# Performance work log

Hardware: AMD Instinct MI355X
Metric: run time of the kernel (lower is better)

The kernel has to match this reference:

```python
import jax, jax.numpy as jnp
import numpy as np

N, NFEAT, NHID, NHEADS, NCLASS = 4096, 64, 64, 4, 64
ALPHA = 0.2        # LeakyReLU negative slope
NEG = -9.0e15      # mask value from the torch code (-9e15)


def _xavier(key, shape, gain=1.414):
    fan_in, fan_out = shape[-2] if len(shape) > 1 else shape[-1], shape[-1]
    if len(shape) == 1:
        fan_in, fan_out = shape[0], 1
    bound = gain * np.sqrt(6.0 / (fan_in + fan_out))
    return jax.random.uniform(key, shape, jnp.float32, -bound, bound)


def setup_inputs() -> dict:
    key = jax.random.key(0)
    ks = jax.random.split(key, 6)
    x = jax.random.normal(ks[0], (N, NFEAT), jnp.float32)
    # sparse-ish adjacency mask with self loops (adj > 0 gating in torch code)
    adj = jax.random.bernoulli(ks[1], 0.02, (N, N)) | jnp.eye(N, dtype=bool)
    W_heads = _xavier(ks[2], (NHEADS, NFEAT, NHID))                  # per-head W
    a_heads = _xavier(ks[3], (NHEADS, 2 * NHID))                     # per-head a (flattened [2F',1])
    W_out = _xavier(ks[4], (NHEADS * NHID, NCLASS))
    a_out = _xavier(ks[5], (2 * NCLASS,))
    return {"x": x, "W_heads": W_heads, "a_heads": a_heads,
            "W_out": W_out, "a_out": a_out, "adj": adj}


def gat_layer(x, adj, W, a, concat):
    # h: [N, F']
    h = x @ W
    Fp = h.shape[-1]
    # e_ij = leakyrelu(a[:F'].h_i + a[F':].h_j)  == torch's cat([h_i, h_j]) @ a
    f1 = h @ a[:Fp]                 # [N]
    f2 = h @ a[Fp:]                 # [N]
    e = jax.nn.leaky_relu(f1[:, None] + f2[None, :], ALPHA)   # [N, N]
    att = jax.nn.softmax(jnp.where(adj, e, NEG), axis=1)      # row softmax over neighbors
    hp = att @ h                    # [N, F']
    return jax.nn.elu(hp) if concat else hp


def reference(x, W_heads, a_heads, W_out, a_out, adj):
    # multi-head GAT with concat (dropout omitted: eval mode)
    heads = jax.vmap(lambda W, a: gat_layer(x, adj, W, a, True))(W_heads, a_heads)  # [H, N, F']
    hcat = jnp.transpose(heads, (1, 0, 2)).reshape(x.shape[0], NHEADS * NHID)       # [N, H*F']
    out = gat_layer(hcat, adj, W_out, a_out, False)                                  # [N, nclass]
    return out
```

## Files before the change

kernel.cpp:

```cpp
#include <hip/hip_runtime.h>
#include <hip/hip_fp16.h>

#define N 4096
#define CAP 160
#define ALPHA 0.2f

__device__ __forceinline__ float wred_sum(float v) {
#pragma unroll
  for (int o = 32; o > 0; o >>= 1) v += __shfl_xor(v, o, 64);
  return v;
}

__device__ __forceinline__ float4 h4_to_f4(float2 raw) {
  union { float2 f2; __half2 h2[2]; } u;
  u.f2 = raw;
  float2 lo = __half22float2(u.h2[0]);
  float2 hi = __half22float2(u.h2[1]);
  return make_float4(lo.x, lo.y, hi.x, hi.y);
}

__global__ void stage1_k(const void* __restrict__ adjv, const float* __restrict__ x,
                         const float* __restrict__ W, const float* __restrict__ a,
                         int* __restrict__ cnt, int* __restrict__ cols,
                         __half* __restrict__ h1, float* __restrict__ f1h,
                         float* __restrict__ f2h) {
  __shared__ float Ws[64 * 64];
  __shared__ float xs[4][64];
  __shared__ int csh;
  int bid = blockIdx.x;
  int tid = threadIdx.x;
  int lane = tid & 63;
  if (bid < N) {
    int i = bid;
    if (tid == 0) csh = 0;
    __syncthreads();
    int* mycols = cols + (size_t)i * CAP;
    const unsigned char* adjB = (const unsigned char*)adjv;
    bool byteLayout = (adjB[(size_t)N + 1] == 1);
    unsigned long long lt = (lane == 0) ? 0ull : (~0ull >> (64 - lane));
    if (!byteLayout) {
      const int4* row = (const int4*)((const int*)adjv + (size_t)i * N);
      int4 v[4];
#pragma unroll
      for (int it = 0; it < 4; ++it) v[it] = row[tid + it * 256];
#pragma unroll
      for (int it = 0; it < 4; ++it) {
        int b = (tid + it * 256) * 4;
        unsigned long long m0 = __ballot(v[it].x != 0);
        unsigned long long m1 = __ballot(v[it].y != 0);
        unsigned long long m2 = __ballot(v[it].z != 0);
        unsigned long long m3 = __ballot(v[it].w != 0);
        int c0 = __popcll(m0), c1 = __popcll(m1), c2 = __popcll(m2);
        int total = c0 + c1 + c2 + __popcll(m3);
        int wb = 0;
        if (lane == 0 && total) wb = atomicAdd(&csh, total);
        wb = __shfl(wb, 0, 64);
        if (v[it].x) { int p = wb + __popcll(m0 & lt); if (p < CAP) mycols[p] = b; }
        if (v[it].y) { int p = wb + c0 + __popcll(m1 & lt); if (p < CAP) mycols[p] = b + 1; }
        if (v[it].z) { int p = wb + c0 + c1 + __popcll(m2 & lt); if (p < CAP) mycols[p] = b + 2; }
        if (v[it].w) { int p = wb + c0 + c1 + c2 + __popcll(m3 & lt); if (p < CAP) mycols[p] = b + 3; }
      }
    } else {
      const unsigned int* row = (const unsigned int*)(adjB + (size_t)i * N);
      unsigned int v[4];
#pragma unroll
      for (int it = 0; it < 4; ++it) v[it] = row[tid + it * 256];
#pragma unroll
      for (int it = 0; it < 4; ++it) {
        int b = (tid + it * 256) * 4;
        unsigned long long m0 = __ballot((v[it] & 0xffu) != 0);
        unsigned long long m1 = __ballot((v[it] & 0xff00u) != 0);
        unsigned long long m2 = __ballot((v[it] & 0xff0000u) != 0);
        unsigned long long m3 = __ballot((v[it] & 0xff000000u) != 0);
        int c0 = __popcll(m0), c1 = __popcll(m1), c2 = __popcll(m2);
        int total = c0 + c1 + c2 + __popcll(m3);
        int wb = 0;
        if (lane == 0 && total) wb = atomicAdd(&csh, total);
        wb = __shfl(wb, 0, 64);
        if (v[it] & 0xffu) { int p = wb + __popcll(m0 & lt); if (p < CAP) mycols[p] = b; }
        if (v[it] & 0xff00u) { int p = wb + c0 + __popcll(m1 & lt); if (p < CAP) mycols[p] = b + 1; }
        if (v[it] & 0xff0000u) { int p = wb + c0 + c1 + __popcll(m2 & lt); if (p < CAP) mycols[p] = b + 2; }
        if (v[it] & 0xff000000u) { int p = wb + c0 + c1 + c2 + __popcll(m3 & lt); if (p < CAP) mycols[p] = b + 3; }
      }
    }
    __syncthreads();
    if (tid == 0) cnt[i] = min(csh, CAP);
  } else {
    int u = bid - N;
    int h = u & 3;
    int r = tid >> 6, f = lane;
    int n = (u >> 2) * 4 + r;
    const float4* W4 = (const float4*)(W + h * 4096);
    float4* Ws4 = (float4*)Ws;
    for (int t = tid; t < 1024; t += 256) Ws4[t] = W4[t];
    xs[r][f] = x[(size_t)n * 64 + f];
    __syncthreads();
    float acc = 0.f;
#pragma unroll
    for (int k = 0; k < 64; ++k) acc = fmaf(xs[r][k], Ws[k * 64 + f], acc);
    h1[((size_t)h * N + n) * 64 + f] = __float2half(acc);
    float s1 = wred_sum(acc * a[h * 128 + f]);
    float s2 = wred_sum(acc * a[h * 128 + 64 + f]);
    if (f == 0) { f1h[n * 4 + h] = s1; f2h[n * 4 + h] = s2; }
  }
}

__global__ void attn1_gemm_k(const int* __restrict__ cnt, const int* __restrict__ cols,
                             const __half* __restrict__ h1,
                             const float* __restrict__ f1g,
                             const float* __restrict__ f2g,
                             const float* __restrict__ Wout,
                             const float* __restrict__ aout,
                             __half* __restrict__ h2, float* __restrict__ f1o,
                             float* __restrict__ f2o) {
  int i = blockIdx.x;
  int tid = threadIdx.x;
  int w = tid >> 6, lane = tid & 63;
  __shared__ int cS[CAP];
  __shared__ float pS[4][CAP];
  __shared__ float red[4][4];
  __shared__ float sDinv[4];
  __shared__ float hrow[256];
  __shared__ float4 part4[4][16];
  int c = cnt[i];
  for (int k = tid; k < c; k += 256) cS[k] = cols[(size_t)i * CAP + k];
  __syncthreads();
  float4 t1 = ((const float4*)f1g)[i];
  float f1i[4] = {t1.x, t1.y, t1.z, t1.w};
  float dloc[4] = {0.f, 0.f, 0.f, 0.f};
  for (int k = tid; k < c; k += 256) {
    float4 t2 = ((const float4*)f2g)[cS[k]];
    float f2v[4] = {t2.x, t2.y, t2.z, t2.w};
#pragma unroll
    for (int h = 0; h < 4; ++h) {
      float s = f1i[h] + f2v[h];
      s = s > 0.f ? s : ALPHA * s;
      float p = __expf(s);
      pS[h][k] = p;
      dloc[h] += p;
    }
  }
#pragma unroll
  for (int h = 0; h < 4; ++h) {
    float d = wred_sum(dloc[h]);
    if (lane == 0) red[w][h] = d;
  }
  __syncthreads();
  if (tid < 4) {
    float d = red[0][tid] + red[1][tid] + red[2][tid] + red[3][tid];
    sDinv[tid] = (c > 0) ? 1.f / d : 0.f;
  }
  __syncthreads();
  int g = lane >> 4, ff = lane & 15, h = w;
  const __half* hb = h1 + ((size_t)h * N) * 64;
  float4 aA = {0.f, 0.f, 0.f, 0.f}, aB = aA, aC = aA, aD = aA;
#pragma unroll 2
  for (int k0 = 0; k0 < c; k0 += 16) {
    int kA = k0 + g, kB = k0 + 4 + g, kC = k0 + 8 + g, kD = k0 + 12 + g;
    bool oA = kA < c, oB = kB < c, oC = kC < c, oD = kD < c;
    int jA = oA ? cS[kA] : 0, jB = oB ? cS[kB] : 0;
    int jC = oC ? cS[kC] : 0, jD = oD ? cS[kD] : 0;
    float pA = oA ? pS[h][kA] : 0.f, pB = oB ? pS[h][kB] : 0.f;
    float pC = oC ? pS[h][kC] : 0.f, pD = oD ? pS[h][kD] : 0.f;
    float2 rA = *(const float2*)(hb + (size_t)jA * 64 + ff * 4);
    float2 rB = *(const float2*)(hb + (size_t)jB * 64 + ff * 4);
    float2 rC = *(const float2*)(hb + (size_t)jC * 64 + ff * 4);
    float2 rD = *(const float2*)(hb + (size_t)jD * 64 + ff * 4);
    float4 vA = h4_to_f4(rA), vB = h4_to_f4(rB);
    float4 vC = h4_to_f4(rC), vD = h4_to_f4(rD);
    aA.x = fmaf(pA, vA.x, aA.x); aA.y = fmaf(pA, vA.y, aA.y);
    aA.z = fmaf(pA, vA.z, aA.z); aA.w = fmaf(pA, vA.w, aA.w);
    aB.x = fmaf(pB, vB.x, aB.x); aB.y = fmaf(pB, vB.y, aB.y);
    aB.z = fmaf(pB, vB.z, aB.z); aB.w = fmaf(pB, vB.w, aB.w);
    aC.x = fmaf(pC, vC.x, aC.x); aC.y = fmaf(pC, vC.y, aC.y);
    aC.z = fmaf(pC, vC.z, aC.z); aC.w = fmaf(pC, vC.w, aC.w);
    aD.x = fmaf(pD, vD.x, aD.x); aD.y = fmaf(pD, vD.y, aD.y);
    aD.z = fmaf(pD, vD.z, aD.z); aD.w = fmaf(pD, vD.w, aD.w);
  }
  float4 acc = {(aA.x + aB.x) + (aC.x + aD.x), (aA.y + aB.y) + (aC.y + aD.y),
                (aA.z + aB.z) + (aC.z + aD.z), (aA.w + aB.w) + (aC.w + aD.w)};
#pragma unroll
  for (int o = 16; o < 64; o <<= 1) {
    acc.x += __shfl_xor(acc.x, o, 64);
    acc.y += __shfl_xor(acc.y, o, 64);
    acc.z += __shfl_xor(acc.z, o, 64);
    acc.w += __shfl_xor(acc.w, o, 64);
  }
  if (g == 0) {
    float dv = sDinv[h];
    float4 v = {acc.x * dv, acc.y * dv, acc.z * dv, acc.w * dv};
    v.x = v.x > 0.f ? v.x : expm1f(v.x);
    v.y = v.y > 0.f ? v.y : expm1f(v.y);
    v.z = v.z > 0.f ? v.z : expm1f(v.z);
    v.w = v.w > 0.f ? v.w : expm1f(v.w);
    *(float4*)(hrow + h * 64 + ff * 4) = v;
  }
  __syncthreads();
  int ko = lane >> 4, f4 = lane & 15;
  float4 wacc = {0.f, 0.f, 0.f, 0.f};
#pragma unroll
  for (int kk = 0; kk < 64; kk += 4) {
    int k = w * 64 + kk + ko;
    float hv = hrow[k];
    float4 wv = *(const float4*)(Wout + (size_t)k * 64 + f4 * 4);
    wacc.x = fmaf(hv, wv.x, wacc.x);
    wacc.y = fmaf(hv, wv.y, wacc.y);
    wacc.z = fmaf(hv, wv.z, wacc.z);
    wacc.w = fmaf(hv, wv.w, wacc.w);
  }
#pragma unroll
  for (int o = 16; o < 64; o <<= 1) {
    wacc.x += __shfl_xor(wacc.x, o, 64);
    wacc.y += __shfl_xor(wacc.y, o, 64);
    wacc.z += __shfl_xor(wacc.z, o, 64);
    wacc.w += __shfl_xor(wacc.w, o, 64);
  }
  if (ko == 0) part4[w][f4] = wacc;
  __syncthreads();
  if (tid < 16) {
    float4 s0 = part4[0][tid], s1_ = part4[1][tid], s2_ = part4[2][tid], s3_ = part4[3][tid];
    float4 s = {(s0.x + s1_.x) + (s2_.x + s3_.x), (s0.y + s1_.y) + (s2_.y + s3_.y),
                (s0.z + s1_.z) + (s2_.z + s3_.z), (s0.w + s1_.w) + (s2_.w + s3_.w)};
    __half2* dst = (__half2*)(h2 + (size_t)i * 64 + tid * 4);
    dst[0] = __floats2half2_rn(s.x, s.y);
    dst[1] = __floats2half2_rn(s.z, s.w);
    float4 a1 = *(const float4*)(aout + tid * 4);
    float4 a2 = *(const float4*)(aout + 64 + tid * 4);
    float s1 = s.x * a1.x + s.y * a1.y + s.z * a1.z + s.w * a1.w;
    float s2 = s.x * a2.x + s.y * a2.y + s.z * a2.z + s.w * a2.w;
#pragma unroll
    for (int o = 1; o < 16; o <<= 1) {
      s1 += __shfl_xor(s1, o, 64);
      s2 += __shfl_xor(s2, o, 64);
    }
    if (tid == 0) { f1o[i] = s1; f2o[i] = s2; }
  }
}

__global__ void attn2_k(const int* __restrict__ cnt, const int* __restrict__ cols,
                        const __half* __restrict__ h2,
                        const float* __restrict__ f1g,
                        const float* __restrict__ f2g,
                        float* __restrict__ outf) {
  int i = blockIdx.x;
  int tid = threadIdx.x;
  int w = tid >> 6, lane = tid & 63;
  __shared__ int cS[CAP];
  __shared__ float pS[CAP];
  __shared__ float red[4];
  __shared__ float sDinv;
  __shared__ float4 part4[4][16];
  int c = cnt[i];
  for (int k = tid; k < c; k += 256) cS[k] = cols[(size_t)i * CAP + k];
  __syncthreads();
  float f1i = f1g[i];
  float dloc = 0.f;
  for (int k = tid; k < c; k += 256) {
    float s = f1i + f2g[cS[k]];
    s = s > 0.f ? s : ALPHA * s;
    float p = __expf(s);
    pS[k] = p;
    dloc += p;
  }
  float d = wred_sum(dloc);
  if (lane == 0) red[w] = d;
  __syncthreads();
  if (tid == 0) {
    float dd = red[0] + red[1] + red[2] + red[3];
    sDinv = (c > 0) ? 1.f / dd : 0.f;
  }
  __syncthreads();
  int g = lane >> 4, ff = lane & 15;
  float4 aA = {0.f, 0.f, 0.f, 0.f}, aB = aA;
#pragma unroll 2
  for (int k0 = 0; k0 < c; k0 += 32) {
    int kA = k0 + w * 4 + g, kB = k0 + 16 + w * 4 + g;
    bool oA = kA < c, oB = kB < c;
    int jA = oA ? cS[kA] : 0, jB = oB ? cS[kB] : 0;
    float pA = oA ? pS[kA] : 0.f, pB = oB ? pS[kB] : 0.f;
    float2 rA = *(const float2*)(h2 + (size_t)jA * 64 + ff * 4);
    float2 rB = *(const float2*)(h2 + (size_t)jB * 64 + ff * 4);
    float4 vA = h4_to_f4(rA), vB = h4_to_f4(rB);
    aA.x = fmaf(pA, vA.x, aA.x); aA.y = fmaf(pA, vA.y, aA.y);
    aA.z = fmaf(pA, vA.z, aA.z); aA.w = fmaf(pA, vA.w, aA.w);
    aB.x = fmaf(pB, vB.x, aB.x); aB.y = fmaf(pB, vB.y, aB.y);
    aB.z = fmaf(pB, vB.z, aB.z); aB.w = fmaf(pB, vB.w, aB.w);
  }
  float4 acc = {aA.x + aB.x, aA.y + aB.y, aA.z + aB.z, aA.w + aB.w};
#pragma unroll
  for (int o = 16; o < 64; o <<= 1) {
    acc.x += __shfl_xor(acc.x, o, 64);
    acc.y += __shfl_xor(acc.y, o, 64);
    acc.z += __shfl_xor(acc.z, o, 64);
    acc.w += __shfl_xor(acc.w, o, 64);
  }
  if (g == 0) part4[w][ff] = acc;
  __syncthreads();
  if (w == 0 && g == 0) {
    float4 p0 = part4[0][ff], p1 = part4[1][ff], p2 = part4[2][ff], p3 = part4[3][ff];
    float inv = sDinv;
    float4 v = {(p0.x + p1.x + p2.x + p3.x) * inv, (p0.y + p1.y + p2.y + p3.y) * inv,
                (p0.z + p1.z + p2.z + p3.z) * inv, (p0.w + p1.w + p2.w + p3.w) * inv};
    *(float4*)(outf + (size_t)i * 64 + ff * 4) = v;
  }
}

extern "C" void kernel_launch(void* const* d_in, const int* in_sizes, int n_in,
                              void* d_out, int out_size, void* d_ws, size_t ws_size,
                              hipStream_t stream) {
  const float* x    = (const float*)d_in[0];
  const float* Wh   = (const float*)d_in[1];
  const float* ah   = (const float*)d_in[2];
  const float* Wout = (const float*)d_in[3];
  const float* aout = (const float*)d_in[4];
  const void*  adj  = d_in[5];

  char* ws = (char*)d_ws;
  int* cnt  = (int*)ws;   ws += (size_t)N * sizeof(int);
  int* cols = (int*)ws;   ws += (size_t)N * CAP * sizeof(int);
  __half* h1 = (__half*)ws; ws += (size_t)N * 256 * sizeof(__half);
  float* f1h  = (float*)ws; ws += (size_t)N * 4 * sizeof(float);
  float* f2h  = (float*)ws; ws += (size_t)N * 4 * sizeof(float);
  __half* h2 = (__half*)ws; ws += (size_t)N * 64 * sizeof(__half);
  float* f1o  = (float*)ws; ws += (size_t)N * sizeof(float);
  float* f2o  = (float*)ws; ws += (size_t)N * sizeof(float);
  (void)in_sizes; (void)n_in; (void)out_size; (void)ws_size;

  stage1_k<<<2 * N, 256, 0, stream>>>(adj, x, Wh, ah, cnt, cols, h1, f1h, f2h);
  attn1_gemm_k<<<N, 256, 0, stream>>>(cnt, cols, h1, f1h, f2h, Wout, aout,
                                      h2, f1o, f2o);
  attn2_k<<<N, 256, 0, stream>>>(cnt, cols, h2, f1o, f2o, (float*)d_out);
}
```

Before: 149.0 us.

## Process multiple rows per block and widen fp16 gathers to 16-byte loads

The projection part of stage1 now handles 16 rows per block, so each 64x64 W tile loaded into shared memory is reused four times, with x values broadcast through shuffles. This cuts that half of the grid from 4096 blocks to 1024. attn1_gemm now processes two destination rows per block, sharing the Wout reads, and both attention kernels gather 8 halfs per lane with float4 loads instead of 4. The intent is to amortize W and Wout traffic and per-block overhead and to cut gather instruction count. In exchange it uses more registers and more shuffle-reduction steps, and a row pair with unequal neighbor counts leaves some lanes idle.

Result: slower. 217.6 us (+46.1%).

```diff
diff --git a/kernel.cpp b/kernel.cpp
--- a/kernel.cpp
+++ b/kernel.cpp
@@ -11,12 +11,15 @@
   return v;
 }
 
-__device__ __forceinline__ float4 h4_to_f4(float2 raw) {
-  union { float2 f2; __half2 h2[2]; } u;
-  u.f2 = raw;
-  float2 lo = __half22float2(u.h2[0]);
-  float2 hi = __half22float2(u.h2[1]);
-  return make_float4(lo.x, lo.y, hi.x, hi.y);
+__device__ __forceinline__ void h8_fma(float4 raw, float p, float* acc) {
+  union { float4 f4; __half2 h2[4]; } u;
+  u.f4 = raw;
+#pragma unroll
+  for (int t = 0; t < 4; ++t) {
+    float2 v = __half22float2(u.h2[t]);
+    acc[2 * t]     = fmaf(p, v.x, acc[2 * t]);
+    acc[2 * t + 1] = fmaf(p, v.y, acc[2 * t + 1]);
+  }
 }
 
 __global__ void stage1_k(const void* __restrict__ adjv, const float* __restrict__ x,
@@ -25,7 +28,6 @@
                          __half* __restrict__ h1, float* __restrict__ f1h,
                          float* __restrict__ f2h) {
   __shared__ float Ws[64 * 64];
-  __shared__ float xs[4][64];
   __shared__ int csh;
   int bid = blockIdx.x;
   int tid = threadIdx.x;
@@ -88,20 +90,33 @@
   } else {
     int u = bid - N;
     int h = u & 3;
+    int rowbase = (u >> 2) * 16;
     int r = tid >> 6, f = lane;
-    int n = (u >> 2) * 4 + r;
     const float4* W4 = (const float4*)(W + h * 4096);
     float4* Ws4 = (float4*)Ws;
     for (int t = tid; t < 1024; t += 256) Ws4[t] = W4[t];
-    xs[r][f] = x[(size_t)n * 64 + f];
+    float xv[4];
+    int n0 = rowbase + r;
+#pragma unroll
+    for (int j = 0; j < 4; ++j) xv[j] = x[(size_t)(n0 + 4 * j) * 64 + f];
     __syncthreads();
-    float acc = 0.f;
-#pragma unroll
-    for (int k = 0; k < 64; ++k) acc = fmaf(xs[r][k], Ws[k * 64 + f], acc);
-    h1[((size_t)h * N + n) * 64 + f] = __float2half(acc);
-    float s1 = wred_sum(acc * a[h * 128 + f]);
-    float s2 = wred_sum(acc * a[h * 128 + 64 + f]);
-    if (f == 0) { f1h[n * 4 + h] = s1; f2h[n * 4 + h] = s2; }
+    float acc[4] = {0.f, 0.f, 0.f, 0.f};
+#pragma unroll
+    for (int k = 0; k < 64; ++k) {
+      float wv = Ws[k * 64 + f];
+#pragma unroll
+      for (int j = 0; j < 4; ++j)
+        acc[j] = fmaf(__shfl(xv[j], k, 64), wv, acc[j]);
+    }
+    float a1v = a[h * 128 + f], a2v = a[h * 128 + 64 + f];
+#pragma unroll
+    for (int j = 0; j < 4; ++j) {
+      int n = n0 + 4 * j;
+      h1[((size_t)h * N + n) * 64 + f] = __float2half(acc[j]);
+      float s1 = wred_sum(acc[j] * a1v);
+      float s2 = wred_sum(acc[j] * a2v);
+      if (f == 0) { f1h[n * 4 + h] = s1; f2h[n * 4 + h] = s2; }
+    }
   }
 }
 
@@ -113,127 +128,132 @@
                              const float* __restrict__ aout,
                              __half* __restrict__ h2, float* __restrict__ f1o,
                              float* __restrict__ f2o) {
-  int i = blockIdx.x;
+  int i0 = blockIdx.x * 2;
+  int i1 = i0 + 1;
   int tid = threadIdx.x;
   int w = tid >> 6, lane = tid & 63;
-  __shared__ int cS[CAP];
-  __shared__ float pS[4][CAP];
-  __shared__ float red[4][4];
-  __shared__ float sDinv[4];
-  __shared__ float hrow[256];
-  __shared__ float4 part4[4][16];
-  int c = cnt[i];
-  for (int k = tid; k < c; k += 256) cS[k] = cols[(size_t)i * CAP + k];
-  __syncthreads();
-  float4 t1 = ((const float4*)f1g)[i];
-  float f1i[4] = {t1.x, t1.y, t1.z, t1.w};
-  float dloc[4] = {0.f, 0.f, 0.f, 0.f};
-  for (int k = tid; k < c; k += 256) {
-    float4 t2 = ((const float4*)f2g)[cS[k]];
-    float f2v[4] = {t2.x, t2.y, t2.z, t2.w};
+  __shared__ int cS[2][CAP];
+  __shared__ float pS[2][4][CAP];
+  __shared__ float red[4][2][4];
+  __shared__ float sDinv[2][4];
+  __shared__ float hrow[2][256];
+  __shared__ float4 part4[2][4][16];
+  int c0 = cnt[i0], c1 = cnt[i1];
+  for (int k = tid; k < c0; k += 256) cS[0][k] = cols[(size_t)i0 * CAP + k];
+  for (int k = tid; k < c1; k += 256) cS[1][k] = cols[(size_t)i1 * CAP + k];
+  __syncthreads();
+  float4 t10 = ((const float4*)f1g)[i0];
+  float4 t11 = ((const float4*)f1g)[i1];
+  float f1r[2][4] = {{t10.x, t10.y, t10.z, t10.w}, {t11.x, t11.y, t11.z, t11.w}};
+  float dloc[2][4] = {{0.f, 0.f, 0.f, 0.f}, {0.f, 0.f, 0.f, 0.f}};
+#pragma unroll
+  for (int rr = 0; rr < 2; ++rr) {
+    int c = rr ? c1 : c0;
+    for (int k = tid; k < c; k += 256) {
+      float4 t2 = ((const float4*)f2g)[cS[rr][k]];
+      float f2v[4] = {t2.x, t2.y, t2.z, t2.w};
+#pragma unroll
+      for (int h = 0; h < 4; ++h) {
+        float s = f1r[rr][h] + f2v[h];
+        s = s > 0.f ? s : ALPHA * s;
+        float p = __expf(s);
+        pS[rr][h][k] = p;
+        dloc[rr][h] += p;
+      }
+    }
+  }
+#pragma unroll
+  for (int rr = 0; rr < 2; ++rr)
 #pragma unroll
     for (int h = 0; h < 4; ++h) {
-      float s = f1i[h] + f2v[h];
-      s = s > 0.f ? s : ALPHA * s;
-      float p = __expf(s);
-      pS[h][k] = p;
-      dloc[h] += p;
-    }
-  }
-#pragma unroll
-  for (int h = 0; h < 4; ++h) {
-    float d = wred_sum(dloc[h]);
-    if (lane == 0) red[w][h] = d;
-  }
-  __syncthreads();
-  if (tid < 4) {
-    float d = red[0][tid] + red[1][tid] + red[2][tid] + red[3][tid];
-    sDinv[tid] = (c > 0) ? 1.f / d : 0.f;
-  }
-  __syncthreads();
-  int g = lane >> 4, ff = lane & 15, h = w;
+      float d = wred_sum(dloc[rr][h]);
+      if (lane == 0) red[w][rr][h] = d;
+    }
+  __syncthreads();
+  if (tid < 8) {
+    int rr = tid >> 2, h = tid & 3;
+    float d = red[0][rr][h] + red[1][rr][h] + red[2][rr][h] + red[3][rr][h];
+    int c = rr ? c1 : c0;
+    sDinv[rr][h] = (c > 0) ? 1.f / d : 0.f;
+  }
+  __syncthreads();
+  int g = lane >> 3, ff = lane & 7, h = w;
   const __half* hb = h1 + ((size_t)h * N) * 64;
-  float4 aA = {0.f, 0.f, 0.f, 0.f}, aB = aA, aC = aA, aD = aA;
+  float a0[8] = {0.f, 0.f, 0.f, 0.f, 0.f, 0.f, 0.f, 0.f};
+  float a1[8] = {0.f, 0.f, 0.f, 0.f, 0.f, 0.f, 0.f, 0.f};
+  int cmax = c0 > c1 ? c0 : c1;
 #pragma unroll 2
-  for (int k0 = 0; k0 < c; k0 += 16) {
-    int kA = k0 + g, kB = k0 + 4 + g, kC = k0 + 8 + g, kD = k0 + 12 + g;
-    bool oA = kA < c, oB = kB < c, oC = kC < c, oD = kD < c;
-    int jA = oA ? cS[kA] : 0, jB = oB ? cS[kB] : 0;
-    int jC = oC ? cS[kC] : 0, jD = oD ? cS[kD] : 0;
-    float pA = oA ? pS[h][kA] : 0.f, pB = oB ? pS[h][kB] : 0.f;
-    float pC = oC ? pS[h][kC] : 0.f, pD = oD ? pS[h][kD] : 0.f;
-    float2 rA = *(const float2*)(hb + (size_t)jA * 64 + ff * 4);
-    float2 rB = *(const float2*)(hb + (size_t)jB * 64 + ff * 4);
-    float2 rC = *(const float2*)(hb + (size_t)jC * 64 + ff * 4);
-    float2 rD = *(const float2*)(hb + (size_t)jD * 64 + ff * 4);
-    float4 vA = h4_to_f4(rA), vB = h4_to_f4(rB);
-    float4 vC = h4_to_f4(rC), vD = h4_to_f4(rD);
-    aA.x = fmaf(pA, vA.x, aA.x); aA.y = fmaf(pA, vA.y, aA.y);
-    aA.z = fmaf(pA, vA.z, aA.z); aA.w = fmaf(pA, vA.w, aA.w);
-    aB.x = fmaf(pB, vB.x, aB.x); aB.y = fmaf(pB, vB.y, aB.y);
-    aB.z = fmaf(pB, vB.z, aB.z); aB.w = fmaf(pB, vB.w, aB.w);
-    aC.x = fmaf(pC, vC.x, aC.x); aC.y = fmaf(pC, vC.y, aC.y);
-    aC.z = fmaf(pC, vC.z, aC.z); aC.w = fmaf(pC, vC.w, aC.w);
-    aD.x = fmaf(pD, vD.x, aD.x); aD.y = fmaf(pD, vD.y, aD.y);
-    aD.z = fmaf(pD, vD.z, aD.z); aD.w = fmaf(pD, vD.w, aD.w);
-  }
-  float4 acc = {(aA.x + aB.x) + (aC.x + aD.x), (aA.y + aB.y) + (aC.y + aD.y),
-                (aA.z + aB.z) + (aC.z + aD.z), (aA.w + aB.w) + (aC.w + aD.w)};
-#pragma unroll
-  for (int o = 16; o < 64; o <<= 1) {
-    acc.x += __shfl_xor(acc.x, o, 64);
-    acc.y += __shfl_xor(acc.y, o, 64);
-    acc.z += __shfl_xor(acc.z, o, 64);
-    acc.w += __shfl_xor(acc.w, o, 64);
-  }
+  for (int k0 = 0; k0 < cmax; k0 += 8) {
+    int k = k0 + g;
+    bool o0 = k < c0, o1 = k < c1;
+    int j0 = o0 ? cS[0][k] : 0, j1 = o1 ? cS[1][k] : 0;
+    float p0 = o0 ? pS[0][h][k] : 0.f, p1 = o1 ? pS[1][h][k] : 0.f;
+    float4 r0 = *(const float4*)(hb + (size_t)j0 * 64 + ff * 8);
+    float4 r1 = *(const float4*)(hb + (size_t)j1 * 64 + ff * 8);
+    h8_fma(r0, p0, a0);
+    h8_fma(r1, p1, a1);
+  }
+#pragma unroll
+  for (int o = 8; o < 64; o <<= 1)
+#pragma unroll
+    for (int e = 0; e < 8; ++e) {
+      a0[e] += __shfl_xor(a0[e], o, 64);
+      a1[e] += __shfl_xor(a1[e], o, 64);
+    }
   if (g == 0) {
-    float dv = sDinv[h];
-    float4 v = {acc.x * dv, acc.y * dv, acc.z * dv, acc.w * dv};
-    v.x = v.x > 0.f ? v.x : expm1f(v.x);
-    v.y = v.y > 0.f ? v.y : expm1f(v.y);
-    v.z = v.z > 0.f ? v.z : expm1f(v.z);
-    v.w = v.w > 0.f ? v.w : expm1f(v.w);
-    *(float4*)(hrow + h * 64 + ff * 4) = v;
+    float d0 = sDinv[0][h], d1 = sDinv[1][h];
+#pragma unroll
+    for (int e = 0; e < 8; ++e) {
+      float v0 = a0[e] * d0;
+      float v1 = a1[e] * d1;
+      v0 = v0 > 0.f ? v0 : expm1f(v0);
+      v1 = v1 > 0.f ? v1 : expm1f(v1);
+      hrow[0][h * 64 + ff * 8 + e] = v0;
+      hrow[1][h * 64 + ff * 8 + e] = v1;
+    }
   }
   __syncthreads();
   int ko = lane >> 4, f4 = lane & 15;
-  float4 wacc = {0.f, 0.f, 0.f, 0.f};
+  float4 wa0 = {0.f, 0.f, 0.f, 0.f}, wa1 = wa0;
 #pragma unroll
   for (int kk = 0; kk < 64; kk += 4) {
     int k = w * 64 + kk + ko;
-    float hv = hrow[k];
     float4 wv = *(const float4*)(Wout + (size_t)k * 64 + f4 * 4);
-    wacc.x = fmaf(hv, wv.x, wacc.x);
-    wacc.y = fmaf(hv, wv.y, wacc.y);
-    wacc.z = fmaf(hv, wv.z, wacc.z);
-    wacc.w = fmaf(hv, wv.w, wacc.w);
+    float h0 = hrow[0][k], h1v = hrow[1][k];
+    wa0.x = fmaf(h0, wv.x, wa0.x); wa0.y = fmaf(h0, wv.y, wa0.y);
+    wa0.z = fmaf(h0, wv.z, wa0.z); wa0.w = fmaf(h0, wv.w, wa0.w);
+    wa1.x = fmaf(h1v, wv.x, wa1.x); wa1.y = fmaf(h1v, wv.y, wa1.y);
+    wa1.z = fmaf(h1v, wv.z, wa1.z); wa1.w = fmaf(h1v, wv.w, wa1.w);
   }
 #pragma unroll
   for (int o = 16; o < 64; o <<= 1) {
-    wacc.x += __shfl_xor(wacc.x, o, 64);
-    wacc.y += __shfl_xor(wacc.y, o, 64);
-    wacc.z += __shfl_xor(wacc.z, o, 64);
-    wacc.w += __shfl_xor(wacc.w, o, 64);
-  }
-  if (ko == 0) part4[w][f4] = wacc;
-  __syncthreads();
-  if (tid < 16) {
-    float4 s0 = part4[0][tid], s1_ = part4[1][tid], s2_ = part4[2][tid], s3_ = part4[3][tid];
+    wa0.x += __shfl_xor(wa0.x, o, 64); wa0.y += __shfl_xor(wa0.y, o, 64);
+    wa0.z += __shfl_xor(wa0.z, o, 64); wa0.w += __shfl_xor(wa0.w, o, 64);
+    wa1.x += __shfl_xor(wa1.x, o, 64); wa1.y += __shfl_xor(wa1.y, o, 64);
+    wa1.z += __shfl_xor(wa1.z, o, 64); wa1.w += __shfl_xor(wa1.w, o, 64);
+  }
+  if (ko == 0) { part4[0][w][f4] = wa0; part4[1][w][f4] = wa1; }
+  __syncthreads();
+  if (tid < 32) {
+    int rr = tid >> 4, fi = tid & 15;
+    float4 s0 = part4[rr][0][fi], s1_ = part4[rr][1][fi];
+    float4 s2_ = part4[rr][2][fi], s3_ = part4[rr][3][fi];
     float4 s = {(s0.x + s1_.x) + (s2_.x + s3_.x), (s0.y + s1_.y) + (s2_.y + s3_.y),
                 (s0.z + s1_.z) + (s2_.z + s3_.z), (s0.w + s1_.w) + (s2_.w + s3_.w)};
-    __half2* dst = (__half2*)(h2 + (size_t)i * 64 + tid * 4);
+    int i = rr ? i1 : i0;
+    __half2* dst = (__half2*)(h2 + (size_t)i * 64 + fi * 4);
     dst[0] = __floats2half2_rn(s.x, s.y);
     dst[1] = __floats2half2_rn(s.z, s.w);
-    float4 a1 = *(const float4*)(aout + tid * 4);
-    float4 a2 = *(const float4*)(aout + 64 + tid * 4);
-    float s1 = s.x * a1.x + s.y * a1.y + s.z * a1.z + s.w * a1.w;
-    float s2 = s.x * a2.x + s.y * a2.y + s.z * a2.z + s.w * a2.w;
+    float4 aA = *(const float4*)(aout + fi * 4);
+    float4 aB = *(const float4*)(aout + 64 + fi * 4);
+    float s1 = s.x * aA.x + s.y * aA.y + s.z * aA.z + s.w * aA.w;
+    float s2 = s.x * aB.x + s.y * aB.y + s.z * aB.z + s.w * aB.w;
 #pragma unroll
     for (int o = 1; o < 16; o <<= 1) {
       s1 += __shfl_xor(s1, o, 64);
       s2 += __shfl_xor(s2, o, 64);
     }
-    if (tid == 0) { f1o[i] = s1; f2o[i] = s2; }
+    if (fi == 0) { f1o[i] = s1; f2o[i] = s2; }
   }
 }
 
@@ -249,7 +269,7 @@
   __shared__ float pS[CAP];
   __shared__ float red[4];
   __shared__ float sDinv;
-  __shared__ float4 part4[4][16];
+  __shared__ float partF[4][64];
   int c = cnt[i];
   for (int k = tid; k < c; k += 256) cS[k] = cols[(size_t)i * CAP + k];
   __syncthreads();
@@ -270,38 +290,28 @@
     sDinv = (c > 0) ? 1.f / dd : 0.f;
   }
   __syncthreads();
-  int g = lane >> 4, ff = lane & 15;
-  float4 aA = {0.f, 0.f, 0.f, 0.f}, aB = aA;
+  int g = lane >> 3, ff = lane & 7;
+  float acc[8] = {0.f, 0.f, 0.f, 0.f, 0.f, 0.f, 0.f, 0.f};
 #pragma unroll 2
   for (int k0 = 0; k0 < c; k0 += 32) {
-    int kA = k0 + w * 4 + g, kB = k0 + 16 + w * 4 + g;
-    bool oA = kA < c, oB = kB < c;
-    int jA = oA ? cS[kA] : 0, jB = oB ? cS[kB] : 0;
-    float pA = oA ? pS[kA] : 0.f, pB = oB ? pS[kB] : 0.f;
-    float2 rA = *(const float2*)(h2 + (size_t)jA * 64 + ff * 4);
-    float2 rB = *(const float2*)(h2 + (size_t)jB * 64 + ff * 4);
-    float4 vA = h4_to_f4(rA), vB = h4_to_f4(rB);
-    aA.x = fmaf(pA, vA.x, aA.x); aA.y = fmaf(pA, vA.y, aA.y);
-    aA.z = fmaf(pA, vA.z, aA.z); aA.w = fmaf(pA, vA.w, aA.w);
-    aB.x = fmaf(pB, vB.x, aB.x); aB.y = fmaf(pB, vB.y, aB.y);
-    aB.z = fmaf(pB, vB.z, aB.z); aB.w = fmaf(pB, vB.w, aB.w);
-  }
-  float4 acc = {aA.x + aB.x, aA.y + aB.y, aA.z + aB.z, aA.w + aB.w};
-#pragma unroll
-  for (int o = 16; o < 64; o <<= 1) {
-    acc.x += __shfl_xor(acc.x, o, 64);
-    acc.y += __shfl_xor(acc.y, o, 64);
-    acc.z += __shfl_xor(acc.z, o, 64);
-    acc.w += __shfl_xor(acc.w, o, 64);
-  }
-  if (g == 0) part4[w][ff] = acc;
-  __syncthreads();
-  if (w == 0 && g == 0) {
-    float4 p0 = part4[0][ff], p1 = part4[1][ff], p2 = part4[2][ff], p3 = part4[3][ff];
-    float inv = sDinv;
-    float4 v = {(p0.x + p1.x + p2.x + p3.x) * inv, (p0.y + p1.y + p2.y + p3.y) * inv,
-                (p0.z + p1.z + p2.z + p3.z) * inv, (p0.w + p1.w + p2.w + p3.w) * inv};
-    *(float4*)(outf + (size_t)i * 64 + ff * 4) = v;
+    int k = k0 + w * 8 + g;
+    bool o = k < c;
+    int j = o ? cS[k] : 0;
+    float p = o ? pS[k] : 0.f;
+    float4 rv = *(const float4*)(h2 + (size_t)j * 64 + ff * 8);
+    h8_fma(rv, p, acc);
+  }
+#pragma unroll
+  for (int o = 8; o < 64; o <<= 1)
+#pragma unroll
+    for (int e = 0; e < 8; ++e) acc[e] += __shfl_xor(acc[e], o, 64);
+  if (g == 0)
+#pragma unroll
+    for (int e = 0; e < 8; ++e) partF[w][ff * 8 + e] = acc[e];
+  __syncthreads();
+  if (tid < 64) {
+    float v = (partF[0][tid] + partF[1][tid] + partF[2][tid] + partF[3][tid]) * sDinv;
+    outf[(size_t)i * 64 + tid] = v;
   }
 }
 
@@ -326,8 +336,8 @@
   float* f2o  = (float*)ws; ws += (size_t)N * sizeof(float);
   (void)in_sizes; (void)n_in; (void)out_size; (void)ws_size;
 
-  stage1_k<<<2 * N, 256, 0, stream>>>(adj, x, Wh, ah, cnt, cols, h1, f1h, f2h);
-  attn1_gemm_k<<<N, 256, 0, stream>>>(cnt, cols, h1, f1h, f2h, Wout, aout,
-                                      h2, f1o, f2o);
+  stage1_k<<<N + 1024, 256, 0, stream>>>(adj, x, Wh, ah, cnt, cols, h1, f1h, f2h);
+  attn1_gemm_k<<<N / 2, 256, 0, stream>>>(cnt, cols, h1, f1h, f2h, Wout, aout,
+                                          h2, f1o, f2o);
   attn2_k<<<N, 256, 0, stream>>>(cnt, cols, h2, f1o, f2o, (float*)d_out);
 }
```
